# Kernel optimization log

Hardware: AMD Instinct MI355X
Metric: run time of the kernel (lower is better)

Reference implementation:

```python
import jax, jax.numpy as jnp
import numpy as np

B, W = 8192, 64
EMBED, NUM_OP = 32, 256


def _extract_features(inst, pc):
    # inst, pc: [B, W] int32 -> [B, W, 12] float32 (matches extract_features)
    f = [
        ((inst >> 28) & 15) / 15.0,
        (inst & 255) / 255.0,
        ((inst >> 16) & 255) / 255.0,
        (pc & 255) / 255.0,
        ((pc >> 8) & 255) / 255.0,
        (inst & 31) / 31.0,
        ((inst >> 5) & 31) / 31.0,
        ((inst >> 30) & 3) / 3.0,
        ((inst >> 26) & 3) / 3.0,
        ((inst >> 31) & 1) * 1.0,
        ((inst >> 10) & 4095) / 4095.0,
        jnp.zeros(inst.shape, jnp.float32),
    ]
    return jnp.stack([x.astype(jnp.float32) for x in f], axis=-1)


def setup_inputs() -> dict:
    key = jax.random.key(0)
    k1, k2, k3, k4 = jax.random.split(key, 4)
    instructions = jax.random.randint(k1, (B, W), 0, 2147483647, dtype=jnp.int32)
    pc = jax.random.randint(k2, (B,), 0, 65536, dtype=jnp.int32)
    opcode_table = jax.random.normal(k3, (NUM_OP, EMBED), dtype=jnp.float32)
    feat_W = jax.random.normal(k4, (12, EMBED), dtype=jnp.float32) * 0.3
    feat_b = jnp.zeros((EMBED,), jnp.float32)
    hazard_weights = jnp.array([5.0, 0.5, 3.0, 5.0, -2.0], jnp.float32)
    return {
        "instructions": instructions,
        "pc": pc,
        "opcode_table": opcode_table,
        "feat_W": feat_W,
        "feat_b": feat_b,
        "hazard_weights": hazard_weights,
    }


def reference(instructions, pc, opcode_table, feat_W, feat_b, hazard_weights):
    b, w = instructions.shape
    pcw = jnp.broadcast_to(pc[:, None], (b, w))

    # encode_instructions (computed as in the torch forward; unused in hybrid path)
    opcodes = (instructions >> 24) & 255
    feats = _extract_features(instructions, pcw)              # [B, W, 12]
    emb = opcode_table[opcodes] + jax.nn.relu(feats @ feat_W + feat_b)  # [B, W, E]
    del emb  # dead in hybrid path (use_hybrid=True default)

    # predict_dependencies_hybrid, fully vectorized over the i<j pairs
    rd = instructions & 31
    rn = (instructions >> 5) & 31
    rm = (instructions >> 16) & 31
    rd_i = rd[:, :, None]  # producer i
    raw = ((rd_i == rn[:, None, :]) | (rd_i == rm[:, None, :])) & (rd_i < 31)
    waw = (rd_i == rd[:, None, :]) & (rd_i < 31) & (rd[:, None, :] < 31)
    score = (hazard_weights[0] * raw.astype(jnp.float32)
             + hazard_weights[2] * waw.astype(jnp.float32)
             + hazard_weights[4])
    upper = jnp.triu(jnp.ones((w, w), jnp.float32), k=1)      # j > i only
    dep_matrix = jax.nn.sigmoid(score) * upper                # [B, W, W]

    # schedule_execution with executed_mask = 0:
    # readiness[:, i] = prod_{j<i} (1 - dep[:, j, i]); dep is 0 for j>=i
    readiness = jnp.prod(1.0 - dep_matrix, axis=1)            # [B, W]
    return dep_matrix, readiness
```

## Files before the change

kernel.cpp:

```cpp
#include <hip/hip_runtime.h>


constexpr int Bv = 8192;
constexpr int Wv = 64;

__global__ __launch_bounds__(256) void ooo_kernel(
    const int* __restrict__ inst,
    const float* __restrict__ hw,
    float* __restrict__ dep,
    float* __restrict__ ready)
{
    const int b   = blockIdx.x;
    const int tid = threadIdx.x;

    __shared__ int   s_rd[Wv], s_rn[Wv], s_rm[Wv];
    __shared__ float s_part[16 * Wv];

    if (tid < Wv) {
        int v = inst[(size_t)b * Wv + tid];
        s_rd[tid] = v & 31;
        s_rn[tid] = (v >> 5) & 31;
        s_rm[tid] = (v >> 16) & 31;
    }

    const float h0 = hw[0], h2 = hw[2], h4 = hw[4];
    const float v00 = 1.f / (1.f + __expf(-(h4)));
    const float v10 = 1.f / (1.f + __expf(-(h0 + h4)));
    const float v01 = 1.f / (1.f + __expf(-(h2 + h4)));
    const float v11 = 1.f / (1.f + __expf(-(h0 + h2 + h4)));

    __syncthreads();

    const int jb = (tid & 15) << 2;
    const int ig = tid >> 4;

    int  rdj[4], rnj[4], rmj[4];
    bool jv[4];
#pragma unroll
    for (int q = 0; q < 4; ++q) {
        rdj[q] = s_rd[jb + q];
        rnj[q] = s_rn[jb + q];
        rmj[q] = s_rm[jb + q];
        jv[q]  = rdj[q] < 31;
    }

    float prod[4] = {1.f, 1.f, 1.f, 1.f};
    float* const dep_row = dep + (size_t)b * Wv * Wv;

#pragma unroll
    for (int k = 0; k < 4; ++k) {
        const int  i   = ig + 16 * k;
        const int  rdi = s_rd[i];
        const bool iv  = rdi < 31;
        float o[4];
#pragma unroll
        for (int q = 0; q < 4; ++q) {
            const int  j   = jb + q;
            const bool raw = iv && ((rdi == rnj[q]) || (rdi == rmj[q]));
            const bool waw = iv && jv[q] && (rdi == rdj[q]);
            float val = waw ? (raw ? v11 : v01) : (raw ? v10 : v00);
            float d   = (j > i) ? val : 0.f;
            o[q] = d;
            prod[q] *= (1.f - d);
        }
        *(float4*)(dep_row + i * Wv + jb) =
            make_float4(o[0], o[1], o[2], o[3]);
    }

    s_part[ig * Wv + jb + 0] = prod[0];
    s_part[ig * Wv + jb + 1] = prod[1];
    s_part[ig * Wv + jb + 2] = prod[2];
    s_part[ig * Wv + jb + 3] = prod[3];
    __syncthreads();

    if (tid < Wv) {
        float r = 1.f;
#pragma unroll
        for (int g = 0; g < 16; ++g) r *= s_part[g * Wv + tid];
        ready[(size_t)b * Wv + tid] = r;
    }
}

extern "C" void kernel_launch(void* const* d_in, const int* in_sizes, int n_in,
                              void* d_out, int out_size, void* d_ws, size_t ws_size,
                              hipStream_t stream) {
    const int*   instructions   = (const int*)d_in[0];
    const float* hazard_weights = (const float*)d_in[5];

    float* dep   = (float*)d_out;
    float* ready = dep + (size_t)Bv * Wv * Wv;

    ooo_kernel<<<Bv, 256, 0, stream>>>(instructions, hazard_weights, dep, ready);
}
```

Baseline: 147.1 us.

## Map one wavefront per batch row using readlane broadcast and nontemporal stores

Restructures the kernel so each 64-lane wavefront handles one batch element, with each lane owning a column j and looping over producers i, reading rd_i through readlane instead of shared memory. This removes the shared-memory staging, both block barriers and the cross-group product reduction, since each lane accumulates its full column product in a register. Stores become per-lane scalar nontemporal writes (coalesced across the wave per row) in place of float4 stores, and the grid shrinks to 4 batches per 256-thread block. The kernel is bound by writing the output, so gains depend on whether the narrower stores and the nontemporal hint keep write bandwidth as high as before.

```diff
diff --git a/kernel.cpp b/kernel.cpp
--- a/kernel.cpp
+++ b/kernel.cpp
@@ -10,18 +10,8 @@
     float* __restrict__ dep,
     float* __restrict__ ready)
 {
-    const int b   = blockIdx.x;
-    const int tid = threadIdx.x;
-
-    __shared__ int   s_rd[Wv], s_rn[Wv], s_rm[Wv];
-    __shared__ float s_part[16 * Wv];
-
-    if (tid < Wv) {
-        int v = inst[(size_t)b * Wv + tid];
-        s_rd[tid] = v & 31;
-        s_rn[tid] = (v >> 5) & 31;
-        s_rm[tid] = (v >> 16) & 31;
-    }
+    const int b    = (blockIdx.x * blockDim.x + threadIdx.x) >> 6;
+    const int lane = threadIdx.x & 63;
 
     const float h0 = hw[0], h2 = hw[2], h4 = hw[4];
     const float v00 = 1.f / (1.f + __expf(-(h4)));
@@ -29,56 +19,27 @@
     const float v01 = 1.f / (1.f + __expf(-(h2 + h4)));
     const float v11 = 1.f / (1.f + __expf(-(h0 + h2 + h4)));
 
-    __syncthreads();
+    const int v   = inst[(size_t)b * Wv + lane];
+    const int rn  = (v >> 5)  & 31;
+    const int rm  = (v >> 16) & 31;
+    const int rd  = v & 31;
+    const int rdv = (rd < 31) ? rd : 64;
 
-    const int jb = (tid & 15) << 2;
-    const int ig = tid >> 4;
+    float prod = 1.f;
+    float* const dep_col = dep + (size_t)b * Wv * Wv + lane;
 
-    int  rdj[4], rnj[4], rmj[4];
-    bool jv[4];
-#pragma unroll
-    for (int q = 0; q < 4; ++q) {
-        rdj[q] = s_rd[jb + q];
-        rnj[q] = s_rn[jb + q];
-        rmj[q] = s_rm[jb + q];
-        jv[q]  = rdj[q] < 31;
+#pragma unroll 8
+    for (int i = 0; i < Wv; ++i) {
+        int rdi = __builtin_amdgcn_readlane(rd, i);
+        rdi = (rdi < 31) ? rdi : 99;
+        const bool raw = (rdi == rn) | (rdi == rm);
+        const bool waw = (rdi == rdv);
+        float d = waw ? (raw ? v11 : v01) : (raw ? v10 : v00);
+        d = (lane > i) ? d : 0.f;
+        __builtin_nontemporal_store(d, dep_col + i * Wv);
+        prod *= (1.f - d);
     }
-
-    float prod[4] = {1.f, 1.f, 1.f, 1.f};
-    float* const dep_row = dep + (size_t)b * Wv * Wv;
-
-#pragma unroll
-    for (int k = 0; k < 4; ++k) {
-        const int  i   = ig + 16 * k;
-        const int  rdi = s_rd[i];
-        const bool iv  = rdi < 31;
-        float o[4];
-#pragma unroll
-        for (int q = 0; q < 4; ++q) {
-            const int  j   = jb + q;
-            const bool raw = iv && ((rdi == rnj[q]) || (rdi == rmj[q]));
-            const bool waw = iv && jv[q] && (rdi == rdj[q]);
-            float val = waw ? (raw ? v11 : v01) : (raw ? v10 : v00);
-            float d   = (j > i) ? val : 0.f;
-            o[q] = d;
-            prod[q] *= (1.f - d);
-        }
-        *(float4*)(dep_row + i * Wv + jb) =
-            make_float4(o[0], o[1], o[2], o[3]);
-    }
-
-    s_part[ig * Wv + jb + 0] = prod[0];
-    s_part[ig * Wv + jb + 1] = prod[1];
-    s_part[ig * Wv + jb + 2] = prod[2];
-    s_part[ig * Wv + jb + 3] = prod[3];
-    __syncthreads();
-
-    if (tid < Wv) {
-        float r = 1.f;
-#pragma unroll
-        for (int g = 0; g < 16; ++g) r *= s_part[g * Wv + tid];
-        ready[(size_t)b * Wv + tid] = r;
-    }
+    ready[(size_t)b * Wv + lane] = prod;
 }
 
 extern "C" void kernel_launch(void* const* d_in, const int* in_sizes, int n_in,
@@ -90,5 +51,6 @@
     float* dep   = (float*)d_out;
     float* ready = dep + (size_t)Bv * Wv * Wv;
 
-    ooo_kernel<<<Bv, 256, 0, stream>>>(instructions, hazard_weights, dep, ready);
+    ooo_kernel<<<(Bv * Wv) / 256, 256, 0, stream>>>(instructions, hazard_weights,
+                                                    dep, ready);
 }
```

After: 151.6 us. 1.03x slower.
